# Optimization experiments

Hardware: AMD Instinct MI355X
Metric: run time of the kernel (lower is better)

Reference implementation:

```python
import jax, jax.numpy as jnp
import numpy as np

TEMP = 1.0  # unique_3D_act_temperature
EPS = 1e-10


def _trilinear_border(vol, gx, gy, gz):
    """grid_sample 5D, mode=bilinear (trilinear), padding=border, align_corners=True.
    vol: [C, D, H, W]; gx/gy/gz: [P] normalized coords in [-1, 1] (x->W, y->H, z->D).
    Returns [C, P]."""
    C, D, H, W = vol.shape
    fx = jnp.clip((gx + 1.0) * 0.5 * (W - 1), 0.0, W - 1)
    fy = jnp.clip((gy + 1.0) * 0.5 * (H - 1), 0.0, H - 1)
    fz = jnp.clip((gz + 1.0) * 0.5 * (D - 1), 0.0, D - 1)
    x0 = jnp.floor(fx).astype(jnp.int32); x1 = jnp.minimum(x0 + 1, W - 1)
    y0 = jnp.floor(fy).astype(jnp.int32); y1 = jnp.minimum(y0 + 1, H - 1)
    z0 = jnp.floor(fz).astype(jnp.int32); z1 = jnp.minimum(z0 + 1, D - 1)
    wx = fx - x0; wy = fy - y0; wz = fz - z0
    def g(zi, yi, xi):
        return vol[:, zi, yi, xi]  # [C, P] gather
    c00 = g(z0, y0, x0) * (1 - wx) + g(z0, y0, x1) * wx
    c01 = g(z0, y1, x0) * (1 - wx) + g(z0, y1, x1) * wx
    c10 = g(z1, y0, x0) * (1 - wx) + g(z1, y0, x1) * wx
    c11 = g(z1, y1, x0) * (1 - wx) + g(z1, y1, x1) * wx
    c0 = c00 * (1 - wy) + c01 * wy
    c1 = c10 * (1 - wy) + c11 * wy
    return c0 * (1 - wz) + c1 * wz


def setup_inputs() -> dict:
    key = jax.random.key(0)
    k1, k2, k3, k4 = jax.random.split(key, 4)
    B, NR, NS = 1, 8192, 128
    Cdim, Ddim, Hd, Wd = 1, 256, 240, 320
    H, W = 480, 640
    fx_, fy_, cx, cy = 500.0, 500.0, W / 2.0, H / 2.0
    intr = jnp.array([[[fx_, 0.0, cx], [0.0, fy_, cy], [0.0, 0.0, 1.0]]], dtype=jnp.float32)
    # back-project random pixels at random depths so projections fall mostly in frame
    u = jax.random.uniform(k1, (B, NR, NS), minval=0.0, maxval=float(W))
    v = jax.random.uniform(k2, (B, NR, NS), minval=0.0, maxval=float(H))
    z = jax.random.uniform(k3, (B, NR, NS), minval=1.1, maxval=10.0)
    pts = jnp.stack([(u - cx) / fx_ * z, (v - cy) / fy_ * z, z], axis=-1).astype(jnp.float32)
    feature_volume = 0.01 * jax.random.normal(k4, (1, Cdim, Ddim, Hd, Wd), dtype=jnp.float32)
    learnable_max_value = 5.0 * jnp.ones((1, 1, 1, Hd, Wd), dtype=jnp.float32)
    return {"feature_volume": feature_volume, "learnable_max_value": learnable_max_value,
            "intr": intr, "points_3D_samples": pts,
            "H": H, "W": W, "depth_min": 0, "depth_max": 1}


def reference(feature_volume, learnable_max_value, intr, points_3D_samples, H, W, depth_min, depth_max):
    B, NR, NS, _ = points_3D_samples.shape
    Cdim = feature_volume.shape[1]
    # camera projection: points @ intr^T
    p2d = jnp.einsum('bnsk,bjk->bnsj', points_3D_samples, intr)
    px, py, pz = p2d[..., 0], p2d[..., 1], p2d[..., 2]
    gx = (px / (pz + EPS) / W - 0.5) * 2.0
    gy = (py / (pz + EPS) / H - 0.5) * 2.0
    gz = ((1.0 / pz - depth_min) / (depth_max - depth_min) - 0.5) * 2.0
    # unique_3D_act density: softmax over depth axis * (relu(max) + 0.01)
    density = jax.nn.softmax(feature_volume * TEMP, axis=2) * (jax.nn.relu(learnable_max_value) + 0.01)
    vol = density[0]  # [C, D, Hd, Wd]
    feat = _trilinear_border(vol, gx.reshape(-1), gy.reshape(-1), gz.reshape(-1))  # [C, P]
    feat = feat.reshape(Cdim, B, NR, NS).transpose(1, 2, 3, 0)  # [B, NR, NS, C]
    density_samples = feat[..., 0]  # cdim == 1 -> squeeze(-1)
    return density_samples
```

## Files before the change

kernel.cpp:

```cpp
#include <hip/hip_runtime.h>
#include <hip/hip_fp16.h>
#include <math.h>

#define DD 256
#define HD 240
#define WD 320
#define HWPIX (HD * WD)
#define DCHUNK 32
#define NCHUNK (DD / DCHUNK)

__global__ __launch_bounds__(256) void k_rebuild(
        const float* __restrict__ vol,
        __half2* __restrict__ pair2,
        float* __restrict__ partial) {
    int pix = blockIdx.x * 256 + threadIdx.x;
    int d0 = blockIdx.y * DCHUNK;
    const float* p = vol + pix;

    float v[DCHUNK + 1];
#pragma unroll
    for (int j = 0; j <= DCHUNK; ++j) {
        int d = d0 + j; if (d > DD - 1) d = DD - 1;
        v[j] = p[(size_t)d * HWPIX];
    }
    float e[DCHUNK + 1];
#pragma unroll
    for (int j = 0; j <= DCHUNK; ++j) e[j] = __expf(v[j]);

    float s0 = 0.f, s1 = 0.f, s2 = 0.f, s3 = 0.f;
#pragma unroll
    for (int j = 0; j < DCHUNK; j += 4) {
        s0 += e[j]; s1 += e[j + 1]; s2 += e[j + 2]; s3 += e[j + 3];
        pair2[(size_t)(d0 + j)     * HWPIX + pix] = __floats2half2_rn(e[j],     e[j + 1]);
        pair2[(size_t)(d0 + j + 1) * HWPIX + pix] = __floats2half2_rn(e[j + 1], e[j + 2]);
        pair2[(size_t)(d0 + j + 2) * HWPIX + pix] = __floats2half2_rn(e[j + 2], e[j + 3]);
        pair2[(size_t)(d0 + j + 3) * HWPIX + pix] = __floats2half2_rn(e[j + 3], e[j + 4]);
    }
    partial[blockIdx.y * HWPIX + pix] = (s0 + s1) + (s2 + s3);
}

__global__ __launch_bounds__(256) void k_stats_partial(
        const float* __restrict__ vol,
        float* __restrict__ partial) {
    int pix = blockIdx.x * 256 + threadIdx.x;
    int d0 = blockIdx.y * DCHUNK;
    const float* p = vol + pix;
    float v[DCHUNK];
#pragma unroll
    for (int j = 0; j < DCHUNK; ++j) v[j] = p[(size_t)(d0 + j) * HWPIX];
    float s0 = 0.f, s1 = 0.f, s2 = 0.f, s3 = 0.f;
#pragma unroll
    for (int j = 0; j < DCHUNK; j += 4) {
        s0 += __expf(v[j]); s1 += __expf(v[j + 1]);
        s2 += __expf(v[j + 2]); s3 += __expf(v[j + 3]);
    }
    partial[blockIdx.y * HWPIX + pix] = (s0 + s1) + (s2 + s3);
}

__global__ __launch_bounds__(256) void k_finalize(
        const float* __restrict__ partial,
        const float* __restrict__ lmax,
        float* __restrict__ coef) {
    int pix = blockIdx.x * 256 + threadIdx.x;
    float s = 0.f;
#pragma unroll
    for (int c = 0; c < NCHUNK; ++c) s += partial[c * HWPIX + pix];
    coef[pix] = (fmaxf(lmax[pix], 0.0f) + 0.01f) / s;
}

__device__ __forceinline__ void project(
        const float* __restrict__ intr, const float* __restrict__ pts, int i,
        float Himg, float Wimg, float dmin, float dmax,
        int& x0, int& x1, float& wx, int& y0, int& y1, float& wy,
        int& z0, float& wz) {
    float X = pts[3 * i + 0];
    float Y = pts[3 * i + 1];
    float Z = pts[3 * i + 2];
    float px = intr[0] * X + intr[1] * Y + intr[2] * Z;
    float py = intr[3] * X + intr[4] * Y + intr[5] * Z;
    float pz = intr[6] * X + intr[7] * Y + intr[8] * Z;
    float inv = 1.0f / (pz + 1e-10f);
    float gx = (px * inv / Wimg - 0.5f) * 2.0f;
    float gy = (py * inv / Himg - 0.5f) * 2.0f;
    float gz = ((1.0f / pz - dmin) / (dmax - dmin) - 0.5f) * 2.0f;
    float fx = fminf(fmaxf((gx + 1.0f) * 0.5f * (float)(WD - 1), 0.0f), (float)(WD - 1));
    float fy = fminf(fmaxf((gy + 1.0f) * 0.5f * (float)(HD - 1), 0.0f), (float)(HD - 1));
    float fz = fminf(fmaxf((gz + 1.0f) * 0.5f * (float)(DD - 1), 0.0f), (float)(DD - 1));
    x0 = (int)floorf(fx); x1 = min(x0 + 1, WD - 1); wx = fx - (float)x0;
    y0 = (int)floorf(fy); y1 = min(y0 + 1, HD - 1); wy = fy - (float)y0;
    z0 = (int)floorf(fz); wz = fz - (float)z0;
}

__global__ __launch_bounds__(256) void k_sample_pair(
        const __half2* __restrict__ pair2,
        const float* __restrict__ coef,
        const float* __restrict__ intr,
        const float* __restrict__ pts,
        const int* __restrict__ Hp, const int* __restrict__ Wp,
        const int* __restrict__ dminp, const int* __restrict__ dmaxp,
        float* __restrict__ out, int P) {
    int i = blockIdx.x * 256 + threadIdx.x;
    if (i >= P) return;
    float Himg = (float)(*Hp), Wimg = (float)(*Wp);
    float dmin = (float)(*dminp), dmax = (float)(*dmaxp);
    int x0, x1, y0, y1, z0; float wx, wy, wz;
    project(intr, pts, i, Himg, Wimg, dmin, dmax, x0, x1, wx, y0, y1, wy, z0, wz);

    int p00 = y0 * WD + x0, p01 = y0 * WD + x1;
    int p10 = y1 * WD + x0, p11 = y1 * WD + x1;

    const __half2* vz = pair2 + (size_t)z0 * HWPIX;
    __half2 h00 = vz[p00], h01 = vz[p01], h10 = vz[p10], h11 = vz[p11];
    float c00 = coef[p00], c01 = coef[p01], c10 = coef[p10], c11 = coef[p11];

    float2 f00 = __half22float2(h00), f01 = __half22float2(h01);
    float2 f10 = __half22float2(h10), f11 = __half22float2(h11);

    float a00 = f00.x * c00, a01 = f01.x * c01, a10 = f10.x * c10, a11 = f11.x * c11;
    float b00 = f00.y * c00, b01 = f01.y * c01, b10 = f10.y * c10, b11 = f11.y * c11;

    float ax0 = a00 * (1.0f - wx) + a01 * wx;
    float ax1 = a10 * (1.0f - wx) + a11 * wx;
    float bx0 = b00 * (1.0f - wx) + b01 * wx;
    float bx1 = b10 * (1.0f - wx) + b11 * wx;
    float a = ax0 * (1.0f - wy) + ax1 * wy;
    float b = bx0 * (1.0f - wy) + bx1 * wy;
    out[i] = a * (1.0f - wz) + b * wz;
}

__global__ __launch_bounds__(256) void k_sample_vol(
        const float* __restrict__ vol,
        const float* __restrict__ coef,
        const float* __restrict__ intr,
        const float* __restrict__ pts,
        const int* __restrict__ Hp, const int* __restrict__ Wp,
        const int* __restrict__ dminp, const int* __restrict__ dmaxp,
        float* __restrict__ out, int P) {
    int i = blockIdx.x * 256 + threadIdx.x;
    if (i >= P) return;
    float Himg = (float)(*Hp), Wimg = (float)(*Wp);
    float dmin = (float)(*dminp), dmax = (float)(*dmaxp);
    int x0, x1, y0, y1, z0; float wx, wy, wz;
    project(intr, pts, i, Himg, Wimg, dmin, dmax, x0, x1, wx, y0, y1, wy, z0, wz);
    int z1 = min(z0 + 1, DD - 1);

    int p00 = y0 * WD + x0, p01 = y0 * WD + x1;
    int p10 = y1 * WD + x0, p11 = y1 * WD + x1;
    float c00 = coef[p00], c01 = coef[p01], c10 = coef[p10], c11 = coef[p11];
    const float* v0 = vol + (size_t)z0 * HWPIX;
    const float* v1 = vol + (size_t)z1 * HWPIX;

    float a00 = __expf(v0[p00]) * c00, a01 = __expf(v0[p01]) * c01;
    float a10 = __expf(v0[p10]) * c10, a11 = __expf(v0[p11]) * c11;
    float b00 = __expf(v1[p00]) * c00, b01 = __expf(v1[p01]) * c01;
    float b10 = __expf(v1[p10]) * c10, b11 = __expf(v1[p11]) * c11;

    float ax0 = a00 * (1.0f - wx) + a01 * wx;
    float ax1 = a10 * (1.0f - wx) + a11 * wx;
    float bx0 = b00 * (1.0f - wx) + b01 * wx;
    float bx1 = b10 * (1.0f - wx) + b11 * wx;
    float a = ax0 * (1.0f - wy) + ax1 * wy;
    float b = bx0 * (1.0f - wy) + bx1 * wy;
    out[i] = a * (1.0f - wz) + b * wz;
}

extern "C" void kernel_launch(void* const* d_in, const int* in_sizes, int n_in,
                              void* d_out, int out_size, void* d_ws, size_t ws_size,
                              hipStream_t stream) {
    const float* vol  = (const float*)d_in[0];
    const float* lmax = (const float*)d_in[1];
    const float* intr = (const float*)d_in[2];
    const float* pts  = (const float*)d_in[3];
    const int* Hp     = (const int*)d_in[4];
    const int* Wp     = (const int*)d_in[5];
    const int* dminp  = (const int*)d_in[6];
    const int* dmaxp  = (const int*)d_in[7];
    float* out = (float*)d_out;
    int P = out_size;

    const size_t pair_bytes = (size_t)DD * HWPIX * sizeof(__half2);
    const size_t part_bytes = (size_t)NCHUNK * HWPIX * 4;
    const size_t coef_bytes = (size_t)HWPIX * 4;

    dim3 blk(256);
    dim3 grd_rb(HWPIX / 256, NCHUNK);
    dim3 grd_fin(HWPIX / 256);
    dim3 grd_smp((P + 255) / 256);

    if (ws_size >= pair_bytes + part_bytes + coef_bytes) {
        __half2* pair2 = (__half2*)d_ws;
        float* partial = (float*)((char*)d_ws + pair_bytes);
        float* coef    = (float*)((char*)d_ws + pair_bytes + part_bytes);
        k_rebuild<<<grd_rb, blk, 0, stream>>>(vol, pair2, partial);
        k_finalize<<<grd_fin, blk, 0, stream>>>(partial, lmax, coef);
        k_sample_pair<<<grd_smp, blk, 0, stream>>>(pair2, coef, intr, pts,
                                                   Hp, Wp, dminp, dmaxp, out, P);
    } else {
        float* partial = (float*)d_ws;
        float* coef    = (float*)((char*)d_ws + part_bytes);
        k_stats_partial<<<grd_rb, blk, 0, stream>>>(vol, partial);
        k_finalize<<<grd_fin, blk, 0, stream>>>(partial, lmax, coef);
        k_sample_vol<<<grd_smp, blk, 0, stream>>>(vol, coef, intr, pts,
                                                  Hp, Wp, dminp, dmaxp, out, P);
    }
}
```

Measured before the change: 179.0 us.

## Pack z and y neighbors into 8-byte quad texels to halve sample gathers

The precomputed exp volume now stores, for each (z, y, x), a quad of half values covering z/z+1 and y/y+1. The sampler then needs only two 8-byte gathers per point instead of four 4-byte gathers. The rebuild kernel reads two rows, uses a smaller depth chunk, and writes twice as many bytes to the workspace. The sampler also processes two points per thread. The cost is a larger intermediate buffer and more rebuild write traffic, traded for fewer random reads during sampling.

```diff
diff --git a/kernel.cpp b/kernel.cpp
--- a/kernel.cpp
+++ b/kernel.cpp
@@ -6,37 +6,47 @@
 #define HD 240
 #define WD 320
 #define HWPIX (HD * WD)
-#define DCHUNK 32
+#define DCHUNK 16
 #define NCHUNK (DD / DCHUNK)
 
-__global__ __launch_bounds__(256) void k_rebuild(
+union Quad {
+    uint2 u;
+    struct { __half2 lo, hi; } h;
+};
+
+__global__ __launch_bounds__(256) void k_rebuild_quad(
         const float* __restrict__ vol,
-        __half2* __restrict__ pair2,
+        uint2* __restrict__ quad,
         float* __restrict__ partial) {
     int pix = blockIdx.x * 256 + threadIdx.x;
     int d0 = blockIdx.y * DCHUNK;
-    const float* p = vol + pix;
-
-    float v[DCHUNK + 1];
+    int y = pix / WD;
+    int pixn = (y < HD - 1) ? pix + WD : pix;
+    const float* p0 = vol + pix;
+    const float* p1 = vol + pixn;
+
+    float a[DCHUNK + 1], b[DCHUNK + 1];
 #pragma unroll
     for (int j = 0; j <= DCHUNK; ++j) {
         int d = d0 + j; if (d > DD - 1) d = DD - 1;
-        v[j] = p[(size_t)d * HWPIX];
-    }
-    float e[DCHUNK + 1];
-#pragma unroll
-    for (int j = 0; j <= DCHUNK; ++j) e[j] = __expf(v[j]);
-
-    float s0 = 0.f, s1 = 0.f, s2 = 0.f, s3 = 0.f;
-#pragma unroll
-    for (int j = 0; j < DCHUNK; j += 4) {
-        s0 += e[j]; s1 += e[j + 1]; s2 += e[j + 2]; s3 += e[j + 3];
-        pair2[(size_t)(d0 + j)     * HWPIX + pix] = __floats2half2_rn(e[j],     e[j + 1]);
-        pair2[(size_t)(d0 + j + 1) * HWPIX + pix] = __floats2half2_rn(e[j + 1], e[j + 2]);
-        pair2[(size_t)(d0 + j + 2) * HWPIX + pix] = __floats2half2_rn(e[j + 2], e[j + 3]);
-        pair2[(size_t)(d0 + j + 3) * HWPIX + pix] = __floats2half2_rn(e[j + 3], e[j + 4]);
-    }
-    partial[blockIdx.y * HWPIX + pix] = (s0 + s1) + (s2 + s3);
+        a[j] = p0[(size_t)d * HWPIX];
+        b[j] = p1[(size_t)d * HWPIX];
+    }
+#pragma unroll
+    for (int j = 0; j <= DCHUNK; ++j) { a[j] = __expf(a[j]); b[j] = __expf(b[j]); }
+
+    float s0 = 0.f, s1 = 0.f;
+#pragma unroll
+    for (int j = 0; j < DCHUNK; j += 2) { s0 += a[j]; s1 += a[j + 1]; }
+
+#pragma unroll
+    for (int j = 0; j < DCHUNK; ++j) {
+        Quad q;
+        q.h.lo = __floats2half2_rn(a[j],     b[j]);
+        q.h.hi = __floats2half2_rn(a[j + 1], b[j + 1]);
+        quad[(size_t)(d0 + j) * HWPIX + pix] = q.u;
+    }
+    partial[blockIdx.y * HWPIX + pix] = s0 + s1;
 }
 
 __global__ __launch_bounds__(256) void k_stats_partial(
@@ -48,13 +58,10 @@
     float v[DCHUNK];
 #pragma unroll
     for (int j = 0; j < DCHUNK; ++j) v[j] = p[(size_t)(d0 + j) * HWPIX];
-    float s0 = 0.f, s1 = 0.f, s2 = 0.f, s3 = 0.f;
-#pragma unroll
-    for (int j = 0; j < DCHUNK; j += 4) {
-        s0 += __expf(v[j]); s1 += __expf(v[j + 1]);
-        s2 += __expf(v[j + 2]); s3 += __expf(v[j + 3]);
-    }
-    partial[blockIdx.y * HWPIX + pix] = (s0 + s1) + (s2 + s3);
+    float s0 = 0.f, s1 = 0.f;
+#pragma unroll
+    for (int j = 0; j < DCHUNK; j += 2) { s0 += __expf(v[j]); s1 += __expf(v[j + 1]); }
+    partial[blockIdx.y * HWPIX + pix] = s0 + s1;
 }
 
 __global__ __launch_bounds__(256) void k_finalize(
@@ -91,41 +98,59 @@
     z0 = (int)floorf(fz); wz = fz - (float)z0;
 }
 
-__global__ __launch_bounds__(256) void k_sample_pair(
-        const __half2* __restrict__ pair2,
+__device__ __forceinline__ float sample_one_quad(
+        const uint2* __restrict__ quad, const float* __restrict__ coef,
+        const float* __restrict__ intr, const float* __restrict__ pts,
+        float Himg, float Wimg, float dmin, float dmax, int i) {
+    int x0, x1, y0, y1, z0; float wx, wy, wz;
+    project(intr, pts, i, Himg, Wimg, dmin, dmax, x0, x1, wx, y0, y1, wy, z0, wz);
+
+    size_t base = (size_t)z0 * HWPIX + (size_t)y0 * WD;
+    Quad qa, qb;
+    qa.u = quad[base + x0];
+    qb.u = quad[base + x1];
+    float c00 = coef[y0 * WD + x0], c01 = coef[y0 * WD + x1];
+    float c10 = coef[y1 * WD + x0], c11 = coef[y1 * WD + x1];
+
+    float2 alo = __half22float2(qa.h.lo);
+    float2 ahi = __half22float2(qa.h.hi);
+    float2 blo = __half22float2(qb.h.lo);
+    float2 bhi = __half22float2(qb.h.hi);
+
+    float d000 = alo.x * c00, d010 = alo.y * c10;
+    float d100 = ahi.x * c00, d110 = ahi.y * c10;
+    float d001 = blo.x * c01, d011 = blo.y * c11;
+    float d101 = bhi.x * c01, d111 = bhi.y * c11;
+
+    float e00 = d000 * (1.0f - wx) + d001 * wx;
+    float e01 = d010 * (1.0f - wx) + d011 * wx;
+    float e10 = d100 * (1.0f - wx) + d101 * wx;
+    float e11 = d110 * (1.0f - wx) + d111 * wx;
+    float f0 = e00 * (1.0f - wy) + e01 * wy;
+    float f1 = e10 * (1.0f - wy) + e11 * wy;
+    return f0 * (1.0f - wz) + f1 * wz;
+}
+
+__global__ __launch_bounds__(256) void k_sample_quad(
+        const uint2* __restrict__ quad,
         const float* __restrict__ coef,
         const float* __restrict__ intr,
         const float* __restrict__ pts,
         const int* __restrict__ Hp, const int* __restrict__ Wp,
         const int* __restrict__ dminp, const int* __restrict__ dmaxp,
-        float* __restrict__ out, int P) {
-    int i = blockIdx.x * 256 + threadIdx.x;
-    if (i >= P) return;
+        float* __restrict__ out, int P, int half) {
+    int t = blockIdx.x * 256 + threadIdx.x;
+    if (t >= half) return;
     float Himg = (float)(*Hp), Wimg = (float)(*Wp);
     float dmin = (float)(*dminp), dmax = (float)(*dmaxp);
-    int x0, x1, y0, y1, z0; float wx, wy, wz;
-    project(intr, pts, i, Himg, Wimg, dmin, dmax, x0, x1, wx, y0, y1, wy, z0, wz);
-
-    int p00 = y0 * WD + x0, p01 = y0 * WD + x1;
-    int p10 = y1 * WD + x0, p11 = y1 * WD + x1;
-
-    const __half2* vz = pair2 + (size_t)z0 * HWPIX;
-    __half2 h00 = vz[p00], h01 = vz[p01], h10 = vz[p10], h11 = vz[p11];
-    float c00 = coef[p00], c01 = coef[p01], c10 = coef[p10], c11 = coef[p11];
-
-    float2 f00 = __half22float2(h00), f01 = __half22float2(h01);
-    float2 f10 = __half22float2(h10), f11 = __half22float2(h11);
-
-    float a00 = f00.x * c00, a01 = f01.x * c01, a10 = f10.x * c10, a11 = f11.x * c11;
-    float b00 = f00.y * c00, b01 = f01.y * c01, b10 = f10.y * c10, b11 = f11.y * c11;
-
-    float ax0 = a00 * (1.0f - wx) + a01 * wx;
-    float ax1 = a10 * (1.0f - wx) + a11 * wx;
-    float bx0 = b00 * (1.0f - wx) + b01 * wx;
-    float bx1 = b10 * (1.0f - wx) + b11 * wx;
-    float a = ax0 * (1.0f - wy) + ax1 * wy;
-    float b = bx0 * (1.0f - wy) + bx1 * wy;
-    out[i] = a * (1.0f - wz) + b * wz;
+
+    int i0 = t, i1 = t + half;
+    float r0 = sample_one_quad(quad, coef, intr, pts, Himg, Wimg, dmin, dmax, i0);
+    out[i0] = r0;
+    if (i1 < P) {
+        float r1 = sample_one_quad(quad, coef, intr, pts, Himg, Wimg, dmin, dmax, i1);
+        out[i1] = r1;
+    }
 }
 
 __global__ __launch_bounds__(256) void k_sample_vol(
@@ -178,28 +203,30 @@
     float* out = (float*)d_out;
     int P = out_size;
 
-    const size_t pair_bytes = (size_t)DD * HWPIX * sizeof(__half2);
+    const size_t quad_bytes = (size_t)DD * HWPIX * sizeof(uint2);
     const size_t part_bytes = (size_t)NCHUNK * HWPIX * 4;
     const size_t coef_bytes = (size_t)HWPIX * 4;
 
     dim3 blk(256);
     dim3 grd_rb(HWPIX / 256, NCHUNK);
     dim3 grd_fin(HWPIX / 256);
-    dim3 grd_smp((P + 255) / 256);
-
-    if (ws_size >= pair_bytes + part_bytes + coef_bytes) {
-        __half2* pair2 = (__half2*)d_ws;
-        float* partial = (float*)((char*)d_ws + pair_bytes);
-        float* coef    = (float*)((char*)d_ws + pair_bytes + part_bytes);
-        k_rebuild<<<grd_rb, blk, 0, stream>>>(vol, pair2, partial);
+
+    if (ws_size >= quad_bytes + part_bytes + coef_bytes) {
+        uint2* quad    = (uint2*)d_ws;
+        float* partial = (float*)((char*)d_ws + quad_bytes);
+        float* coef    = (float*)((char*)d_ws + quad_bytes + part_bytes);
+        k_rebuild_quad<<<grd_rb, blk, 0, stream>>>(vol, quad, partial);
         k_finalize<<<grd_fin, blk, 0, stream>>>(partial, lmax, coef);
-        k_sample_pair<<<grd_smp, blk, 0, stream>>>(pair2, coef, intr, pts,
-                                                   Hp, Wp, dminp, dmaxp, out, P);
+        int half = (P + 1) / 2;
+        dim3 grd_smp((half + 255) / 256);
+        k_sample_quad<<<grd_smp, blk, 0, stream>>>(quad, coef, intr, pts,
+                                                   Hp, Wp, dminp, dmaxp, out, P, half);
     } else {
         float* partial = (float*)d_ws;
         float* coef    = (float*)((char*)d_ws + part_bytes);
         k_stats_partial<<<grd_rb, blk, 0, stream>>>(vol, partial);
         k_finalize<<<grd_fin, blk, 0, stream>>>(partial, lmax, coef);
+        dim3 grd_smp((P + 255) / 256);
         k_sample_vol<<<grd_smp, blk, 0, stream>>>(vol, coef, intr, pts,
                                                   Hp, Wp, dminp, dmaxp, out, P);
     }
```

Result: slower. 194.1 us (+8.4%).
